# Performance work log

Measured on AMD Instinct MI355X. Metric: run time of the kernel, lower is better.

Reference implementation:

```python
import jax, jax.numpy as jnp
import numpy as np

B = 131072
LATENT = 64
ACTION = 2
HID = 256


def setup_inputs() -> dict:
    key = jax.random.key(0)
    ks = jax.random.split(key, 10)
    s = lambda fan_in: 1.0 / np.sqrt(fan_in)
    return {
        "z": jax.random.normal(ks[0], (B, LATENT), jnp.float32),
        "action": jax.random.normal(ks[1], (B, ACTION), jnp.float32),
        "hidden": jax.random.normal(ks[2], (1, B, HID), jnp.float32),
        "W_in": jax.random.normal(ks[3], (HID, LATENT + ACTION), jnp.float32) * s(LATENT + ACTION),
        "b_in": jnp.zeros((HID,), jnp.float32),
        "W_ih": jax.random.normal(ks[4], (3 * HID, HID), jnp.float32) * s(HID),
        "W_hh": jax.random.normal(ks[5], (3 * HID, HID), jnp.float32) * s(HID),
        "b_ih": jnp.zeros((3 * HID,), jnp.float32),
        "b_hh": jnp.zeros((3 * HID,), jnp.float32),
        "W_o1": jax.random.normal(ks[6], (HID, HID), jnp.float32) * s(HID),
        "b_o1": jnp.zeros((HID,), jnp.float32),
        "W_o2": jax.random.normal(ks[7], (LATENT, HID), jnp.float32) * s(HID),
        "b_o2": jnp.zeros((LATENT,), jnp.float32),
    }


def reference(z, action, hidden, W_in, b_in, W_ih, W_hh, b_ih, b_hh, W_o1, b_o1, W_o2, b_o2):
    # input projection: Linear + ReLU on concat([z, action])
    x = jnp.concatenate([z, action], axis=-1)          # [B, latent+action]
    x = jax.nn.relu(x @ W_in.T + b_in)                 # [B, H]
    # single-step GRU cell (PyTorch gate order: r, z, n)
    h = hidden[0]                                      # [B, H]
    gi = x @ W_ih.T + b_ih                             # [B, 3H]
    gh = h @ W_hh.T + b_hh                             # [B, 3H]
    i_r, i_z, i_n = jnp.split(gi, 3, axis=-1)
    h_r, h_z, h_n = jnp.split(gh, 3, axis=-1)
    r = jax.nn.sigmoid(i_r + h_r)
    zg = jax.nn.sigmoid(i_z + h_z)
    n = jnp.tanh(i_n + r * h_n)
    h_new = (1.0 - zg) * n + zg * h                    # [B, H]
    # output projection: Linear + ReLU + Linear
    y = jax.nn.relu(h_new @ W_o1.T + b_o1)
    z_next = y @ W_o2.T + b_o2                         # [B, latent]
    return z_next, h_new[None]                         # hidden shape (1, B, H)
```

## Files before the change

kernel.cpp:

```cpp
#include <hip/hip_runtime.h>


typedef unsigned short u16;
typedef unsigned int u32;
using bf16x8 = __attribute__((ext_vector_type(8))) short;
using f32x4  = __attribute__((ext_vector_type(4))) float;
using u16x4  = __attribute__((ext_vector_type(4))) unsigned short;

constexpr int B_TOT = 131072;
constexpr int BM    = 64;

constexpr int OFF_WIN = 0;
constexpr int OFF_WG  = 16384;
constexpr int OFF_WO1 = 409600;
constexpr int OFF_WO2 = 475136;
constexpr int WS_TOT  = 491520;

__device__ __forceinline__ u16 f2b(float f) {
    u32 u = __builtin_bit_cast(u32, f);
    return (u16)((u + 0x7FFFu + ((u >> 16) & 1u)) >> 16);
}
__device__ __forceinline__ u32 pkbf(float lo, float hi) {
    u32 r;
    asm("v_cvt_pk_bf16_f32 %0, %1, %2" : "=v"(r) : "v"(lo), "v"(hi));
    return r;
}
__device__ __forceinline__ float sigm(float x) {
    x = fminf(fmaxf(x, -30.f), 30.f);
    float e = __expf(x);
    return e * __builtin_amdgcn_rcpf(1.f + e);
}
__device__ __forceinline__ float tanh_(float x) {
    x = fminf(fmaxf(x, -15.f), 15.f);
    float e = __expf(2.f * x);
    return (e - 1.f) * __builtin_amdgcn_rcpf(e + 1.f);
}
__device__ __forceinline__ bf16x8 ld8f_bf(const float* __restrict__ p) {
    float4 a = *reinterpret_cast<const float4*>(p);
    float4 b = *reinterpret_cast<const float4*>(p + 4);
    union { u32 u[4]; bf16x8 v; } q;
    q.u[0] = pkbf(a.x, a.y); q.u[1] = pkbf(a.z, a.w);
    q.u[2] = pkbf(b.x, b.y); q.u[3] = pkbf(b.z, b.w);
    return q.v;
}
__device__ __forceinline__ float b2f(u16 u) {
    u32 x = (u32)u << 16;
    return __builtin_bit_cast(float, x);
}
__device__ __forceinline__ int fidx(int row, int kv) {
    return ((row >> 4) * 16 + (kv >> 5)) * 512 + ((kv >> 3) & 3) * 128 + (row & 15) * 8 + (kv & 7);
}

#define MFMA(a, b, c) __builtin_amdgcn_mfma_f32_16x16x32_bf16((a), (b), (c), 0, 0, 0)

__global__ void ldm_prep(const float* __restrict__ W_in, const float* __restrict__ W_ih,
                         const float* __restrict__ W_hh, const float* __restrict__ W_o1,
                         const float* __restrict__ W_o2, u16* __restrict__ ws)
{
    int i = blockIdx.x * blockDim.x + threadIdx.x;
    if (i >= WS_TOT) return;
    const int lane = (i >> 3) & 63;
    const int e    = i & 7;
    const int lrow = lane & 15;
    const int kq   = (lane >> 4) * 8 + e;
    float v;
    if (i < OFF_WG) {
        const int blk = i >> 9;
        const int kc = blk & 1, t = blk >> 1;
        v = W_in[(t * 16 + lrow) * 66 + kc * 32 + kq];
    } else if (i < OFF_WO1) {
        const int j = i - OFF_WG;
        const int blk = j >> 9;
        const int kc16 = blk & 15, gt = blk >> 4;
        const int g = gt >> 4, t = gt & 15;
        const int grow = g * 256 + t * 16 + lrow;
        const int k = (kc16 & 7) * 32 + kq;
        v = (kc16 < 8) ? W_ih[grow * 256 + k] : W_hh[grow * 256 + k];
    } else if (i < OFF_WO2) {
        const int j = i - OFF_WO1;
        const int blk = j >> 9;
        const int kc = blk & 7, t = blk >> 3;
        v = W_o1[(t * 16 + lrow) * 256 + kc * 32 + kq];
    } else {
        const int j = i - OFF_WO2;
        const int blk = j >> 9;
        const int kc = blk & 7, t = blk >> 3;
        v = W_o2[(t * 16 + lrow) * 256 + kc * 32 + kq];
    }
    ws[i] = f2b(v);
}

__global__ __launch_bounds__(512, 4)
void ldm_fused(const float* __restrict__ z, const float* __restrict__ act,
               const float* __restrict__ hid,
               const float* __restrict__ W_in_f, const float* __restrict__ b_in,
               const float* __restrict__ b_ih, const float* __restrict__ b_hh,
               const float* __restrict__ b_o1, const float* __restrict__ b_o2,
               const u16* __restrict__ ws,
               float* __restrict__ zn_out, float* __restrict__ h_out)
{
    __shared__ u16 xh[4 * 16 * 512];

    const int tid  = threadIdx.x;
    const int w    = tid >> 6;
    const int lane = tid & 63;
    const int l16  = lane & 15;
    const int quad = lane >> 4;
    const int row0 = blockIdx.x * BM;
    const int lofs = lane * 8;

    const int hr  = tid >> 3;
    const int hc0 = (tid & 7) * 32;
    float4 hreg[8];
    {
        const float* hp = hid + (size_t)(row0 + hr) * 256 + hc0;
        #pragma unroll
        for (int i = 0; i < 8; ++i)
            hreg[i] = reinterpret_cast<const float4*>(hp)[i];
    }

    {
        bf16x8 az[4][2];
        #pragma unroll
        for (int mt = 0; mt < 4; ++mt) {
            const float* zp = z + (size_t)(row0 + mt * 16 + l16) * 64 + quad * 8;
            az[mt][0] = ld8f_bf(zp);
            az[mt][1] = ld8f_bf(zp + 32);
        }
        #pragma unroll
        for (int ot = 0; ot < 2; ++ot) {
            const int T = w * 2 + ot;
            const int orow = T * 16 + l16;
            bf16x8 bw[2];
            #pragma unroll
            for (int kc = 0; kc < 2; ++kc)
                bw[kc] = *reinterpret_cast<const bf16x8*>(ws + OFF_WIN + (T * 2 + kc) * 512 + lofs);
            f32x4 acc[4];
            #pragma unroll
            for (int mt = 0; mt < 4; ++mt) acc[mt] = {0.f, 0.f, 0.f, 0.f};
            #pragma unroll
            for (int kc = 0; kc < 2; ++kc)
                #pragma unroll
                for (int mt = 0; mt < 4; ++mt)
                    acc[mt] = MFMA(az[mt][kc], bw[kc], acc[mt]);
            const float w64v = W_in_f[orow * 66 + 64];
            const float w65v = W_in_f[orow * 66 + 65];
            const float bi   = b_in[orow];
            #pragma unroll
            for (int mt = 0; mt < 4; ++mt) {
                #pragma unroll
                for (int i = 0; i < 4; ++i) {
                    const int rl = mt * 16 + quad * 4 + i;
                    const float2 av = reinterpret_cast<const float2*>(act)[row0 + rl];
                    float v = acc[mt][i] + av.x * w64v + av.y * w65v + bi;
                    xh[fidx(rl, orow)] = f2b(fmaxf(v, 0.f));
                }
            }
        }
    }

    {
        #pragma unroll
        for (int i = 0; i < 8; ++i) {
            union { u32 u[2]; u16x4 v; } q;
            q.u[0] = pkbf(hreg[i].x, hreg[i].y);
            q.u[1] = pkbf(hreg[i].z, hreg[i].w);
            *reinterpret_cast<u16x4*>(&xh[fidx(hr, 256 + hc0 + i * 4)]) = q.v;
        }
    }
    __syncthreads();

    u32 hnp0[8], hnp1[8];

    auto gru_tile = [&](const int ot, u32 (&pk)[8]) {
        const int T = w * 2 + ot;
        const int o = T * 16 + l16;
        const u16* WR = ws + OFF_WG + (size_t)((0  + T) * 16) * 512 + lofs;
        const u16* WZ = ws + OFF_WG + (size_t)((16 + T) * 16) * 512 + lofs;
        const u16* WN = ws + OFF_WG + (size_t)((32 + T) * 16) * 512 + lofs;

        f32x4 gR[4], gZ[4], gNi[4], gNh[4];
        #pragma unroll
        for (int mt = 0; mt < 4; ++mt) {
            gR[mt]  = {0.f, 0.f, 0.f, 0.f};
            gZ[mt]  = {0.f, 0.f, 0.f, 0.f};
            gNi[mt] = {0.f, 0.f, 0.f, 0.f};
            gNh[mt] = {0.f, 0.f, 0.f, 0.f};
        }

        auto step = [&](const int kc, const bf16x8& wr_, const bf16x8& wz_,
                        const bf16x8& wn_, f32x4 (&gNt)[4]) {
            bf16x8 a0 = *reinterpret_cast<const bf16x8*>(&xh[(0 * 16 + kc) * 512 + lofs]);
            bf16x8 a1 = *reinterpret_cast<const bf16x8*>(&xh[(1 * 16 + kc) * 512 + lofs]);
            gR[0]  = MFMA(a0, wr_, gR[0]);
            gZ[0]  = MFMA(a0, wz_, gZ[0]);
            gNt[0] = MFMA(a0, wn_, gNt[0]);
            gR[1]  = MFMA(a1, wr_, gR[1]);
            gZ[1]  = MFMA(a1, wz_, gZ[1]);
            gNt[1] = MFMA(a1, wn_, gNt[1]);
            bf16x8 a2 = *reinterpret_cast<const bf16x8*>(&xh[(2 * 16 + kc) * 512 + lofs]);
            bf16x8 a3 = *reinterpret_cast<const bf16x8*>(&xh[(3 * 16 + kc) * 512 + lofs]);
            gR[2]  = MFMA(a2, wr_, gR[2]);
            gZ[2]  = MFMA(a2, wz_, gZ[2]);
            gNt[2] = MFMA(a2, wn_, gNt[2]);
            gR[3]  = MFMA(a3, wr_, gR[3]);
            gZ[3]  = MFMA(a3, wz_, gZ[3]);
            gNt[3] = MFMA(a3, wn_, gNt[3]);
        };

        #pragma unroll
        for (int k2 = 0; k2 < 8; ++k2) {
            const int kc0 = k2 * 2, kc1 = kc0 + 1;
            bf16x8 wr0 = *reinterpret_cast<const bf16x8*>(WR + kc0 * 512);
            bf16x8 wz0 = *reinterpret_cast<const bf16x8*>(WZ + kc0 * 512);
            bf16x8 wn0 = *reinterpret_cast<const bf16x8*>(WN + kc0 * 512);
            bf16x8 wr1 = *reinterpret_cast<const bf16x8*>(WR + kc1 * 512);
            bf16x8 wz1 = *reinterpret_cast<const bf16x8*>(WZ + kc1 * 512);
            bf16x8 wn1 = *reinterpret_cast<const bf16x8*>(WN + kc1 * 512);
            if (k2 < 4) {
                step(kc0, wr0, wz0, wn0, gNi);
                step(kc1, wr1, wz1, wn1, gNi);
            } else {
                step(kc0, wr0, wz0, wn0, gNh);
                step(kc1, wr1, wz1, wn1, gNh);
            }
        }

        const float br_b = b_ih[o]       + b_hh[o];
        const float bz_b = b_ih[o + 256] + b_hh[o + 256];
        const float bni  = b_ih[o + 512];
        const float bnh  = b_hh[o + 512];
        #pragma unroll
        for (int mt = 0; mt < 4; ++mt) {
            float hn[4];
            #pragma unroll
            for (int i = 0; i < 4; ++i) {
                const int rl = mt * 16 + quad * 4 + i;
                const float hv = b2f(xh[fidx(rl, 256 + o)]);
                const float r  = sigm(gR[mt][i] + br_b);
                const float zg = sigm(gZ[mt][i] + bz_b);
                const float n  = tanh_(gNi[mt][i] + bni + r * (gNh[mt][i] + bnh));
                hn[i] = n + zg * (hv - n);
            }
            pk[mt * 2]     = pkbf(hn[0], hn[1]);
            pk[mt * 2 + 1] = pkbf(hn[2], hn[3]);
        }
    };

    gru_tile(0, hnp0);
    __builtin_amdgcn_sched_barrier(0);
    gru_tile(1, hnp1);

    __syncthreads();

    auto scat = [&](const int ot, const u32 (&pk)[8]) {
        const int o = (w * 2 + ot) * 16 + l16;
        #pragma unroll
        for (int mt = 0; mt < 4; ++mt) {
            #pragma unroll
            for (int p = 0; p < 2; ++p) {
                const u32 v = pk[mt * 2 + p];
                const int rl = mt * 16 + quad * 4 + p * 2;
                xh[fidx(rl,     256 + o)] = (u16)v;
                xh[fidx(rl + 1, 256 + o)] = (u16)(v >> 16);
            }
        }
    };
    scat(0, hnp0);
    scat(1, hnp1);
    __syncthreads();

    #pragma unroll
    for (int it = 0; it < 4; ++it) {
        const int idx = it * 4096 + tid * 8;
        const int r = idx >> 8, c = idx & 255;
        const bf16x8 v = *reinterpret_cast<const bf16x8*>(&xh[fidx(r, 256 + c)]);
        float4 f0, f1;
        f0.x = b2f((u16)v[0]); f0.y = b2f((u16)v[1]); f0.z = b2f((u16)v[2]); f0.w = b2f((u16)v[3]);
        f1.x = b2f((u16)v[4]); f1.y = b2f((u16)v[5]); f1.z = b2f((u16)v[6]); f1.w = b2f((u16)v[7]);
        float* dst = h_out + (size_t)(row0 + r) * 256 + c;
        *reinterpret_cast<float4*>(dst)     = f0;
        *reinterpret_cast<float4*>(dst + 4) = f1;
    }

    #pragma unroll 1
    for (int ot = 0; ot < 2; ++ot) {
        const int T = w * 2 + ot;
        const int o = T * 16 + l16;
        f32x4 aY[4];
        #pragma unroll
        for (int mt = 0; mt < 4; ++mt) aY[mt] = {0.f, 0.f, 0.f, 0.f};
        bf16x8 wo[8];
        #pragma unroll
        for (int kc = 0; kc < 8; ++kc)
            wo[kc] = *reinterpret_cast<const bf16x8*>(ws + OFF_WO1 + (T * 8 + kc) * 512 + lofs);
        #pragma unroll
        for (int kc = 0; kc < 8; ++kc) {
            bf16x8 ah2[4];
            #pragma unroll
            for (int mt = 0; mt < 4; ++mt)
                ah2[mt] = *reinterpret_cast<const bf16x8*>(&xh[(mt * 16 + 8 + kc) * 512 + lofs]);
            #pragma unroll
            for (int mt = 0; mt < 4; ++mt)
                aY[mt] = MFMA(ah2[mt], wo[kc], aY[mt]);
        }
        const float bo1 = b_o1[o];
        #pragma unroll
        for (int mt = 0; mt < 4; ++mt)
            #pragma unroll
            for (int i = 0; i < 4; ++i) {
                const int rl = mt * 16 + quad * 4 + i;
                xh[fidx(rl, o)] = f2b(fmaxf(aY[mt][i] + bo1, 0.f));
            }
    }
    __syncthreads();

    {
        const int colt = w & 3;
        const int rh   = w >> 2;
        const int o = colt * 16 + l16;
        f32x4 aO[2];
        aO[0] = {0.f, 0.f, 0.f, 0.f};
        aO[1] = {0.f, 0.f, 0.f, 0.f};
        bf16x8 wo2[8];
        #pragma unroll
        for (int kc = 0; kc < 8; ++kc)
            wo2[kc] = *reinterpret_cast<const bf16x8*>(ws + OFF_WO2 + (colt * 8 + kc) * 512 + lofs);
        #pragma unroll
        for (int kc = 0; kc < 8; ++kc) {
            bf16x8 ay[2];
            #pragma unroll
            for (int mt = 0; mt < 2; ++mt)
                ay[mt] = *reinterpret_cast<const bf16x8*>(&xh[((rh * 2 + mt) * 16 + kc) * 512 + lofs]);
            aO[0] = MFMA(ay[0], wo2[kc], aO[0]);
            aO[1] = MFMA(ay[1], wo2[kc], aO[1]);
        }
        const float bz2 = b_o2[o];

        __syncthreads();
        float* zsc = reinterpret_cast<float*>(xh);
        #pragma unroll
        for (int mt = 0; mt < 2; ++mt)
            #pragma unroll
            for (int i = 0; i < 4; ++i) {
                const int rl = rh * 32 + mt * 16 + quad * 4 + i;
                zsc[rl * 68 + o] = aO[mt][i] + bz2;
            }
        __syncthreads();
        const int zr = tid >> 3, zc = (tid & 7) * 8;
        float4 z0 = *reinterpret_cast<const float4*>(&zsc[zr * 68 + zc]);
        float4 z1 = *reinterpret_cast<const float4*>(&zsc[zr * 68 + zc + 4]);
        float* dst = zn_out + (size_t)(row0 + zr) * 64 + zc;
        *reinterpret_cast<float4*>(dst)     = z0;
        *reinterpret_cast<float4*>(dst + 4) = z1;
    }
}

extern "C" void kernel_launch(void* const* d_in, const int* in_sizes, int n_in,
                              void* d_out, int out_size, void* d_ws, size_t ws_size,
                              hipStream_t stream) {
    const float* z    = (const float*)d_in[0];
    const float* act  = (const float*)d_in[1];
    const float* hid  = (const float*)d_in[2];
    const float* W_in = (const float*)d_in[3];
    const float* b_in = (const float*)d_in[4];
    const float* W_ih = (const float*)d_in[5];
    const float* W_hh = (const float*)d_in[6];
    const float* b_ih = (const float*)d_in[7];
    const float* b_hh = (const float*)d_in[8];
    const float* W_o1 = (const float*)d_in[9];
    const float* b_o1 = (const float*)d_in[10];
    const float* W_o2 = (const float*)d_in[11];
    const float* b_o2 = (const float*)d_in[12];

    u16* ws = (u16*)d_ws;

    float* zn_out = (float*)d_out;
    float* h_out  = zn_out + (size_t)B_TOT * 64;

    ldm_prep<<<dim3((WS_TOT + 255) / 256), dim3(256), 0, stream>>>(
        W_in, W_ih, W_hh, W_o1, W_o2, ws);

    ldm_fused<<<dim3(B_TOT / BM), dim3(512), 0, stream>>>(
        z, act, hid, W_in, b_in, b_ih, b_hh, b_o1, b_o2, ws, zn_out, h_out);
}
```

Baseline: 450.4 us.

## Halve block to 4 waves, each computing two GRU tiles per A-fragment load

```diff
diff --git a/kernel.cpp b/kernel.cpp
--- a/kernel.cpp
+++ b/kernel.cpp
@@ -90,7 +90,7 @@
     ws[i] = f2b(v);
 }
 
-__global__ __launch_bounds__(512, 4)
+__global__ __launch_bounds__(256, 2)
 void ldm_fused(const float* __restrict__ z, const float* __restrict__ act,
                const float* __restrict__ hid,
                const float* __restrict__ W_in_f, const float* __restrict__ b_in,
@@ -109,14 +109,15 @@
     const int row0 = blockIdx.x * BM;
     const int lofs = lane * 8;
 
-    const int hr  = tid >> 3;
-    const int hc0 = (tid & 7) * 32;
-    float4 hreg[8];
+    const int hr  = tid >> 2;
+    const int hc0 = (tid & 3) * 64;
+    float4 hregA[8], hregB[8];
     {
         const float* hp = hid + (size_t)(row0 + hr) * 256 + hc0;
         #pragma unroll
-        for (int i = 0; i < 8; ++i)
-            hreg[i] = reinterpret_cast<const float4*>(hp)[i];
+        for (int i = 0; i < 8; ++i) hregA[i] = reinterpret_cast<const float4*>(hp)[i];
+        #pragma unroll
+        for (int i = 0; i < 8; ++i) hregB[i] = reinterpret_cast<const float4*>(hp)[8 + i];
     }
 
     {
@@ -128,8 +129,8 @@
             az[mt][1] = ld8f_bf(zp + 32);
         }
         #pragma unroll
-        for (int ot = 0; ot < 2; ++ot) {
-            const int T = w * 2 + ot;
+        for (int ot = 0; ot < 4; ++ot) {
+            const int T = w * 4 + ot;
             const int orow = T * 16 + l16;
             bf16x8 bw[2];
             #pragma unroll
@@ -163,69 +164,25 @@
         #pragma unroll
         for (int i = 0; i < 8; ++i) {
             union { u32 u[2]; u16x4 v; } q;
-            q.u[0] = pkbf(hreg[i].x, hreg[i].y);
-            q.u[1] = pkbf(hreg[i].z, hreg[i].w);
+            q.u[0] = pkbf(hregA[i].x, hregA[i].y);
+            q.u[1] = pkbf(hregA[i].z, hregA[i].w);
             *reinterpret_cast<u16x4*>(&xh[fidx(hr, 256 + hc0 + i * 4)]) = q.v;
         }
+        #pragma unroll
+        for (int i = 0; i < 8; ++i) {
+            union { u32 u[2]; u16x4 v; } q;
+            q.u[0] = pkbf(hregB[i].x, hregB[i].y);
+            q.u[1] = pkbf(hregB[i].z, hregB[i].w);
+            *reinterpret_cast<u16x4*>(&xh[fidx(hr, 256 + hc0 + 32 + i * 4)]) = q.v;
+        }
     }
     __syncthreads();
 
-    u32 hnp0[8], hnp1[8];
-
-    auto gru_tile = [&](const int ot, u32 (&pk)[8]) {
-        const int T = w * 2 + ot;
+    u32 hnpA[8], hnpB[8], hnpC[8], hnpD[8];
+
+    auto epi = [&](const int T, const f32x4 (&R)[4], const f32x4 (&Zg)[4],
+                   const f32x4 (&Ni)[4], const f32x4 (&Nh)[4], u32 (&pk)[8]) {
         const int o = T * 16 + l16;
-        const u16* WR = ws + OFF_WG + (size_t)((0  + T) * 16) * 512 + lofs;
-        const u16* WZ = ws + OFF_WG + (size_t)((16 + T) * 16) * 512 + lofs;
-        const u16* WN = ws + OFF_WG + (size_t)((32 + T) * 16) * 512 + lofs;
-
-        f32x4 gR[4], gZ[4], gNi[4], gNh[4];
-        #pragma unroll
-        for (int mt = 0; mt < 4; ++mt) {
-            gR[mt]  = {0.f, 0.f, 0.f, 0.f};
-            gZ[mt]  = {0.f, 0.f, 0.f, 0.f};
-            gNi[mt] = {0.f, 0.f, 0.f, 0.f};
-            gNh[mt] = {0.f, 0.f, 0.f, 0.f};
-        }
-
-        auto step = [&](const int kc, const bf16x8& wr_, const bf16x8& wz_,
-                        const bf16x8& wn_, f32x4 (&gNt)[4]) {
-            bf16x8 a0 = *reinterpret_cast<const bf16x8*>(&xh[(0 * 16 + kc) * 512 + lofs]);
-            bf16x8 a1 = *reinterpret_cast<const bf16x8*>(&xh[(1 * 16 + kc) * 512 + lofs]);
-            gR[0]  = MFMA(a0, wr_, gR[0]);
-            gZ[0]  = MFMA(a0, wz_, gZ[0]);
-            gNt[0] = MFMA(a0, wn_, gNt[0]);
-            gR[1]  = MFMA(a1, wr_, gR[1]);
-            gZ[1]  = MFMA(a1, wz_, gZ[1]);
-            gNt[1] = MFMA(a1, wn_, gNt[1]);
-            bf16x8 a2 = *reinterpret_cast<const bf16x8*>(&xh[(2 * 16 + kc) * 512 + lofs]);
-            bf16x8 a3 = *reinterpret_cast<const bf16x8*>(&xh[(3 * 16 + kc) * 512 + lofs]);
-            gR[2]  = MFMA(a2, wr_, gR[2]);
-            gZ[2]  = MFMA(a2, wz_, gZ[2]);
-            gNt[2] = MFMA(a2, wn_, gNt[2]);
-            gR[3]  = MFMA(a3, wr_, gR[3]);
-            gZ[3]  = MFMA(a3, wz_, gZ[3]);
-            gNt[3] = MFMA(a3, wn_, gNt[3]);
-        };
-
-        #pragma unroll
-        for (int k2 = 0; k2 < 8; ++k2) {
-            const int kc0 = k2 * 2, kc1 = kc0 + 1;
-            bf16x8 wr0 = *reinterpret_cast<const bf16x8*>(WR + kc0 * 512);
-            bf16x8 wz0 = *reinterpret_cast<const bf16x8*>(WZ + kc0 * 512);
-            bf16x8 wn0 = *reinterpret_cast<const bf16x8*>(WN + kc0 * 512);
-            bf16x8 wr1 = *reinterpret_cast<const bf16x8*>(WR + kc1 * 512);
-            bf16x8 wz1 = *reinterpret_cast<const bf16x8*>(WZ + kc1 * 512);
-            bf16x8 wn1 = *reinterpret_cast<const bf16x8*>(WN + kc1 * 512);
-            if (k2 < 4) {
-                step(kc0, wr0, wz0, wn0, gNi);
-                step(kc1, wr1, wz1, wn1, gNi);
-            } else {
-                step(kc0, wr0, wz0, wn0, gNh);
-                step(kc1, wr1, wz1, wn1, gNh);
-            }
-        }
-
         const float br_b = b_ih[o]       + b_hh[o];
         const float bz_b = b_ih[o + 256] + b_hh[o + 256];
         const float bni  = b_ih[o + 512];
@@ -237,9 +194,9 @@
             for (int i = 0; i < 4; ++i) {
                 const int rl = mt * 16 + quad * 4 + i;
                 const float hv = b2f(xh[fidx(rl, 256 + o)]);
-                const float r  = sigm(gR[mt][i] + br_b);
-                const float zg = sigm(gZ[mt][i] + bz_b);
-                const float n  = tanh_(gNi[mt][i] + bni + r * (gNh[mt][i] + bnh));
+                const float r  = sigm(R[mt][i] + br_b);
+                const float zg = sigm(Zg[mt][i] + bz_b);
+                const float n  = tanh_(Ni[mt][i] + bni + r * (Nh[mt][i] + bnh));
                 hn[i] = n + zg * (hv - n);
             }
             pk[mt * 2]     = pkbf(hn[0], hn[1]);
@@ -247,14 +204,63 @@
         }
     };
 
-    gru_tile(0, hnp0);
-    __builtin_amdgcn_sched_barrier(0);
-    gru_tile(1, hnp1);
+    auto gru_pair = [&](const int p, u32 (&pk0)[8], u32 (&pk1)[8]) {
+        const int T0 = w * 4 + p * 2;
+        const int T1 = T0 + 1;
+        const u16* WR0 = ws + OFF_WG + (size_t)((0  + T0) * 16) * 512 + lofs;
+        const u16* WR1 = ws + OFF_WG + (size_t)((0  + T1) * 16) * 512 + lofs;
+        const u16* WZ0 = ws + OFF_WG + (size_t)((16 + T0) * 16) * 512 + lofs;
+        const u16* WZ1 = ws + OFF_WG + (size_t)((16 + T1) * 16) * 512 + lofs;
+        const u16* WN0 = ws + OFF_WG + (size_t)((32 + T0) * 16) * 512 + lofs;
+        const u16* WN1 = ws + OFF_WG + (size_t)((32 + T1) * 16) * 512 + lofs;
+
+        f32x4 gR[2][4], gZ[2][4], gNi[2][4], gNh[2][4];
+        #pragma unroll
+        for (int tt = 0; tt < 2; ++tt)
+            #pragma unroll
+            for (int mt = 0; mt < 4; ++mt) {
+                gR[tt][mt]  = {0.f, 0.f, 0.f, 0.f};
+                gZ[tt][mt]  = {0.f, 0.f, 0.f, 0.f};
+                gNi[tt][mt] = {0.f, 0.f, 0.f, 0.f};
+                gNh[tt][mt] = {0.f, 0.f, 0.f, 0.f};
+            }
+
+        #pragma unroll
+        for (int kc = 0; kc < 16; ++kc) {
+            const bf16x8 wr0 = *reinterpret_cast<const bf16x8*>(WR0 + kc * 512);
+            const bf16x8 wr1 = *reinterpret_cast<const bf16x8*>(WR1 + kc * 512);
+            const bf16x8 wz0 = *reinterpret_cast<const bf16x8*>(WZ0 + kc * 512);
+            const bf16x8 wz1 = *reinterpret_cast<const bf16x8*>(WZ1 + kc * 512);
+            const bf16x8 wn0 = *reinterpret_cast<const bf16x8*>(WN0 + kc * 512);
+            const bf16x8 wn1 = *reinterpret_cast<const bf16x8*>(WN1 + kc * 512);
+            #pragma unroll
+            for (int mt = 0; mt < 4; ++mt) {
+                const bf16x8 am = *reinterpret_cast<const bf16x8*>(&xh[(mt * 16 + kc) * 512 + lofs]);
+                gR[0][mt] = MFMA(am, wr0, gR[0][mt]);
+                gR[1][mt] = MFMA(am, wr1, gR[1][mt]);
+                gZ[0][mt] = MFMA(am, wz0, gZ[0][mt]);
+                gZ[1][mt] = MFMA(am, wz1, gZ[1][mt]);
+                if (kc < 8) {
+                    gNi[0][mt] = MFMA(am, wn0, gNi[0][mt]);
+                    gNi[1][mt] = MFMA(am, wn1, gNi[1][mt]);
+                } else {
+                    gNh[0][mt] = MFMA(am, wn0, gNh[0][mt]);
+                    gNh[1][mt] = MFMA(am, wn1, gNh[1][mt]);
+                }
+            }
+        }
+
+        epi(T0, gR[0], gZ[0], gNi[0], gNh[0], pk0);
+        epi(T1, gR[1], gZ[1], gNi[1], gNh[1], pk1);
+    };
+
+    gru_pair(0, hnpA, hnpB);
+    gru_pair(1, hnpC, hnpD);
 
     __syncthreads();
 
-    auto scat = [&](const int ot, const u32 (&pk)[8]) {
-        const int o = (w * 2 + ot) * 16 + l16;
+    auto scat = [&](const int q, const u32 (&pk)[8]) {
+        const int o = (w * 4 + q) * 16 + l16;
         #pragma unroll
         for (int mt = 0; mt < 4; ++mt) {
             #pragma unroll
@@ -266,13 +272,15 @@
             }
         }
     };
-    scat(0, hnp0);
-    scat(1, hnp1);
+    scat(0, hnpA);
+    scat(1, hnpB);
+    scat(2, hnpC);
+    scat(3, hnpD);
     __syncthreads();
 
     #pragma unroll
-    for (int it = 0; it < 4; ++it) {
-        const int idx = it * 4096 + tid * 8;
+    for (int it = 0; it < 8; ++it) {
+        const int idx = it * 2048 + tid * 8;
         const int r = idx >> 8, c = idx & 255;
         const bf16x8 v = *reinterpret_cast<const bf16x8*>(&xh[fidx(r, 256 + c)]);
         float4 f0, f1;
@@ -284,8 +292,8 @@
     }
 
     #pragma unroll 1
-    for (int ot = 0; ot < 2; ++ot) {
-        const int T = w * 2 + ot;
+    for (int ot = 0; ot < 4; ++ot) {
+        const int T = w * 4 + ot;
         const int o = T * 16 + l16;
         f32x4 aY[4];
         #pragma unroll
@@ -316,43 +324,41 @@
     __syncthreads();
 
     {
-        const int colt = w & 3;
-        const int rh   = w >> 2;
-        const int o = colt * 16 + l16;
-        f32x4 aO[2];
-        aO[0] = {0.f, 0.f, 0.f, 0.f};
-        aO[1] = {0.f, 0.f, 0.f, 0.f};
+        const int o = w * 16 + l16;
+        f32x4 aO[4];
+        #pragma unroll
+        for (int mt = 0; mt < 4; ++mt) aO[mt] = {0.f, 0.f, 0.f, 0.f};
         bf16x8 wo2[8];
         #pragma unroll
         for (int kc = 0; kc < 8; ++kc)
-            wo2[kc] = *reinterpret_cast<const bf16x8*>(ws + OFF_WO2 + (colt * 8 + kc) * 512 + lofs);
+            wo2[kc] = *reinterpret_cast<const bf16x8*>(ws + OFF_WO2 + (w * 8 + kc) * 512 + lofs);
         #pragma unroll
         for (int kc = 0; kc < 8; ++kc) {
-            bf16x8 ay[2];
-            #pragma unroll
-            for (int mt = 0; mt < 2; ++mt)
-                ay[mt] = *reinterpret_cast<const bf16x8*>(&xh[((rh * 2 + mt) * 16 + kc) * 512 + lofs]);
-            aO[0] = MFMA(ay[0], wo2[kc], aO[0]);
-            aO[1] = MFMA(ay[1], wo2[kc], aO[1]);
+            #pragma unroll
+            for (int mt = 0; mt < 4; ++mt) {
+                const bf16x8 ay = *reinterpret_cast<const bf16x8*>(&xh[(mt * 16 + kc) * 512 + lofs]);
+                aO[mt] = MFMA(ay, wo2[kc], aO[mt]);
+            }
         }
         const float bz2 = b_o2[o];
 
         __syncthreads();
         float* zsc = reinterpret_cast<float*>(xh);
         #pragma unroll
-        for (int mt = 0; mt < 2; ++mt)
+        for (int mt = 0; mt < 4; ++mt)
             #pragma unroll
             for (int i = 0; i < 4; ++i) {
-                const int rl = rh * 32 + mt * 16 + quad * 4 + i;
+                const int rl = mt * 16 + quad * 4 + i;
                 zsc[rl * 68 + o] = aO[mt][i] + bz2;
             }
         __syncthreads();
-        const int zr = tid >> 3, zc = (tid & 7) * 8;
-        float4 z0 = *reinterpret_cast<const float4*>(&zsc[zr * 68 + zc]);
-        float4 z1 = *reinterpret_cast<const float4*>(&zsc[zr * 68 + zc + 4]);
+        const int zr = tid >> 2, zc = (tid & 3) * 16;
         float* dst = zn_out + (size_t)(row0 + zr) * 64 + zc;
-        *reinterpret_cast<float4*>(dst)     = z0;
-        *reinterpret_cast<float4*>(dst + 4) = z1;
+        #pragma unroll
+        for (int j = 0; j < 4; ++j) {
+            float4 zv = *reinterpret_cast<const float4*>(&zsc[zr * 68 + zc + j * 4]);
+            *reinterpret_cast<float4*>(dst + j * 4) = zv;
+        }
     }
 }
 
@@ -381,6 +387,6 @@
     ldm_prep<<<dim3((WS_TOT + 255) / 256), dim3(256), 0, stream>>>(
         W_in, W_ih, W_hh, W_o1, W_o2, ws);
 
-    ldm_fused<<<dim3(B_TOT / BM), dim3(512), 0, stream>>>(
+    ldm_fused<<<dim3(B_TOT / BM), dim3(256), 0, stream>>>(
         z, act, hid, W_in, b_in, b_ih, b_hh, b_o1, b_o2, ws, zn_out, h_out);
 }
```

After: 804.5 us. +78.6%, slower.
